# Performance work log

Hardware: AMD Instinct MI355X
Metric: run time of the kernel (lower is better)

Reference implementation:

```python
import jax, jax.numpy as jnp
import numpy as np

B, T, C, H = 16, 2048, 1024, 64

def setup_inputs() -> dict:
    key = jax.random.key(0)
    kx, kq, kk, kv = jax.random.split(key, 4)
    s = 0.02
    return {
        "x": jax.random.normal(kx, (B, T, C), dtype=jnp.float32),
        "Wq": jax.random.normal(kq, (C, H), dtype=jnp.float32) * s,
        "Wk": jax.random.normal(kk, (C, H), dtype=jnp.float32) * s,
        "Wv": jax.random.normal(kv, (C, H), dtype=jnp.float32) * s,
    }

def reference(x, Wq, Wk, Wv):
    Bc, Tc, Cc = x.shape
    q = x @ Wq  # [B,T,H]
    k = x @ Wk  # [B,T,H]
    v = x @ Wv  # [B,T,H]
    # NOTE: original scales by n_embed^{-0.5} (C), not head_size^{-0.5}
    wei = jnp.einsum("bth,bsh->bts", q, k) * (Cc ** -0.5)  # [B,T,T]
    causal = jnp.tril(jnp.ones((Tc, Tc), dtype=bool))
    wei = jnp.where(causal, wei, -jnp.inf)
    wei = jax.nn.softmax(wei, axis=-1)
    # dropout is identity in eval mode
    out = jnp.einsum("bts,bsh->bth", wei, v)  # [B,T,H]
    return out
```

## Files before the change

kernel.cpp:

```cpp
#include <hip/hip_runtime.h>

typedef __attribute__((ext_vector_type(8))) short short8;
typedef __attribute__((ext_vector_type(4))) float float4v;

__device__ inline short f2bf(float f) {
    union { float f; unsigned int u; } c; c.f = f;
    unsigned int u = c.u;
    unsigned int r = (u + 0x7fffu + ((u >> 16) & 1u)) >> 16;
    return (short)r;
}

__global__ __launch_bounds__(256) void wconv_kernel(
    const float* __restrict__ Wq, const float* __restrict__ Wk,
    const float* __restrict__ Wv, short* __restrict__ Wt)
{
    const int n = blockIdx.x;
    const float* W = (n < 64) ? Wq : (n < 128) ? Wk : Wv;
    const int c = n & 63;
#pragma unroll
    for (int i = 0; i < 4; i++) {
        int k = threadIdx.x + i * 256;
        Wt[n * 1024 + k] = f2bf(W[(size_t)k * 64 + c]);
    }
}

#define QSTR 72

__global__ __launch_bounds__(256) void qkv_kernel(
    const float* __restrict__ x, const short* __restrict__ Wt,
    short* __restrict__ qo, short* __restrict__ ko, short* __restrict__ vT)
{
    __shared__ short As[64 * QSTR];
    __shared__ short Bs[192 * QSTR];

    const int tid  = threadIdx.x;
    const int wave = tid >> 6, lane = tid & 63;
    const int quad = lane >> 4, l16 = lane & 15;
    const int m0   = blockIdx.x * 64;

    float4v acc[12];
#pragma unroll
    for (int i = 0; i < 12; i++) acc[i] = (float4v)0.0f;

    const int arow = tid >> 2;
    const int acol = (tid & 3) * 16;

    for (int kc = 0; kc < 1024; kc += 64) {
        __syncthreads();
        {
            const float* src = &x[(size_t)(m0 + arow) * 1024 + kc + acol];
            float4 a0 = ((const float4*)src)[0];
            float4 a1 = ((const float4*)src)[1];
            float4 a2 = ((const float4*)src)[2];
            float4 a3 = ((const float4*)src)[3];
            short8 v0, v1;
            v0[0]=f2bf(a0.x); v0[1]=f2bf(a0.y); v0[2]=f2bf(a0.z); v0[3]=f2bf(a0.w);
            v0[4]=f2bf(a1.x); v0[5]=f2bf(a1.y); v0[6]=f2bf(a1.z); v0[7]=f2bf(a1.w);
            v1[0]=f2bf(a2.x); v1[1]=f2bf(a2.y); v1[2]=f2bf(a2.z); v1[3]=f2bf(a2.w);
            v1[4]=f2bf(a3.x); v1[5]=f2bf(a3.y); v1[6]=f2bf(a3.z); v1[7]=f2bf(a3.w);
            *(short8*)&As[arow * QSTR + acol]     = v0;
            *(short8*)&As[arow * QSTR + acol + 8] = v1;
        }
#pragma unroll
        for (int i = 0; i < 6; i++) {
            int c  = tid + i * 256;
            int n  = c >> 3;
            int k8 = (c & 7) * 8;
            *(short8*)&Bs[n * QSTR + k8] =
                *(const short8*)&Wt[n * 1024 + kc + k8];
        }
        __syncthreads();
#pragma unroll
        for (int kc2 = 0; kc2 < 2; kc2++) {
            short8 af = *(const short8*)&As[(wave*16 + l16) * QSTR + kc2*32 + quad*8];
#pragma unroll
            for (int nt = 0; nt < 12; nt++) {
                short8 bf = *(const short8*)&Bs[(nt*16 + l16) * QSTR + kc2*32 + quad*8];
                acc[nt] = __builtin_amdgcn_mfma_f32_16x16x32_bf16(af, bf, acc[nt], 0, 0, 0);
            }
        }
    }
#pragma unroll
    for (int nt = 0; nt < 8; nt++) {
        short* dst = (nt < 4) ? qo : ko;
        int h = (nt & 3) * 16 + l16;
#pragma unroll
        for (int r = 0; r < 4; r++) {
            int row = m0 + wave*16 + quad*4 + r;
            dst[(size_t)row * 64 + h] = f2bf(acc[nt][r]);
        }
    }
#pragma unroll
    for (int nt = 8; nt < 12; nt++) {
        int h = (nt & 3) * 16 + l16;
#pragma unroll
        for (int r = 0; r < 4; r++) {
            int row = m0 + wave*16 + quad*4 + r;
            int bb = row >> 11, tt = row & 2047;
            vT[((size_t)bb * 64 + h) * 2048 + tt] = f2bf(acc[nt][r]);
        }
    }
}

#define DSTR 72
#define SCALE_LOG2E 0.04508422132f

__global__ __launch_bounds__(256) void attn_kernel(
    const short* __restrict__ q, const short* __restrict__ k,
    const short* __restrict__ vT, float* __restrict__ out)
{
    __shared__ short Ks [64 * DSTR];
    __shared__ short VsT[64 * DSTR];
    __shared__ short Ps [64 * DSTR];

    const int tid  = threadIdx.x;
    const int wave = tid >> 6, lane = tid & 63;
    const int quad = lane >> 4, l16 = lane & 15;
    const int b  = blockIdx.x >> 5;
    const int qt = blockIdx.x & 31;

    const short* kb  = k  + (size_t)b * 2048 * 64;
    const short* vTb = vT + (size_t)b * 64 * 2048;

    const short* qrow = q + ((size_t)b * 2048 + qt*64 + wave*16 + l16) * 64;
    short8 qf0 = *(const short8*)&qrow[quad*8];
    short8 qf1 = *(const short8*)&qrow[32 + quad*8];

    float4v oacc[4];
#pragma unroll
    for (int t = 0; t < 4; t++) oacc[t] = (float4v)0.0f;
    float l_i[4] = {0.f, 0.f, 0.f, 0.f};

    const int tg = qt*64 + wave*16 + quad*4;

    for (int j = 0; j <= qt; j++) {
        __syncthreads();
#pragma unroll
        for (int i = 0; i < 2; i++) {
            int c = tid + i * 256;
            int s = c >> 3, d8 = (c & 7) * 8;
            *(short8*)&Ks[s * DSTR + d8] =
                *(const short8*)&kb[(size_t)(j*64 + s) * 64 + d8];
        }
#pragma unroll
        for (int i = 0; i < 2; i++) {
            int c = tid + i * 256;
            int d = c >> 3, s8 = (c & 7) * 8;
            *(short8*)&VsT[d * DSTR + s8] =
                *(const short8*)&vTb[(size_t)d * 2048 + j*64 + s8];
        }
        __syncthreads();

        float4v sacc[4];
#pragma unroll
        for (int t = 0; t < 4; t++) sacc[t] = (float4v)0.0f;
#pragma unroll
        for (int t = 0; t < 4; t++) {
            short8 bf0 = *(const short8*)&Ks[(t*16 + l16) * DSTR + quad*8];
            short8 bf1 = *(const short8*)&Ks[(t*16 + l16) * DSTR + 32 + quad*8];
            sacc[t] = __builtin_amdgcn_mfma_f32_16x16x32_bf16(qf0, bf0, sacc[t], 0, 0, 0);
            sacc[t] = __builtin_amdgcn_mfma_f32_16x16x32_bf16(qf1, bf1, sacc[t], 0, 0, 0);
        }
        if (j == qt) {
#pragma unroll
            for (int t = 0; t < 4; t++) {
                int sg = j*64 + t*16 + l16;
#pragma unroll
                for (int r = 0; r < 4; r++) {
                    float p = exp2f(sacc[t][r] * SCALE_LOG2E);
                    if (sg > tg + r) p = 0.0f;
                    sacc[t][r] = p;
                    l_i[r] += p;
                }
            }
        } else {
#pragma unroll
            for (int t = 0; t < 4; t++)
#pragma unroll
                for (int r = 0; r < 4; r++) {
                    float p = exp2f(sacc[t][r] * SCALE_LOG2E);
                    sacc[t][r] = p;
                    l_i[r] += p;
                }
        }
#pragma unroll
        for (int t = 0; t < 4; t++)
#pragma unroll
            for (int r = 0; r < 4; r++)
                Ps[(wave*16 + quad*4 + r) * DSTR + t*16 + l16] = f2bf(sacc[t][r]);
#pragma unroll
        for (int kc = 0; kc < 2; kc++) {
            short8 af = *(const short8*)&Ps[(wave*16 + l16) * DSTR + kc*32 + quad*8];
#pragma unroll
            for (int t = 0; t < 4; t++) {
                short8 bf = *(const short8*)&VsT[(t*16 + l16) * DSTR + kc*32 + quad*8];
                oacc[t] = __builtin_amdgcn_mfma_f32_16x16x32_bf16(af, bf, oacc[t], 0, 0, 0);
            }
        }
    }
#pragma unroll
    for (int off = 1; off < 16; off <<= 1)
#pragma unroll
        for (int r = 0; r < 4; r++)
            l_i[r] += __shfl_xor(l_i[r], off, 64);
#pragma unroll
    for (int r = 0; r < 4; r++) {
        float inv = 1.0f / l_i[r];
        int row = qt*64 + wave*16 + quad*4 + r;
#pragma unroll
        for (int t = 0; t < 4; t++)
            out[((size_t)b * 2048 + row) * 64 + t*16 + l16] = oacc[t][r] * inv;
    }
}

extern "C" void kernel_launch(void* const* d_in, const int* in_sizes, int n_in,
                              void* d_out, int out_size, void* d_ws, size_t ws_size,
                              hipStream_t stream)
{
    const float* x  = (const float*)d_in[0];
    const float* Wq = (const float*)d_in[1];
    const float* Wk = (const float*)d_in[2];
    const float* Wv = (const float*)d_in[3];

    short* qw = (short*)d_ws;
    short* kw = qw + (size_t)32768 * 64;
    short* vT = kw + (size_t)32768 * 64;
    short* Wt = vT + (size_t)32768 * 64;
    float* out = (float*)d_out;

    hipLaunchKernelGGL(wconv_kernel, dim3(192), dim3(256), 0, stream,
                       Wq, Wk, Wv, Wt);
    hipLaunchKernelGGL(qkv_kernel, dim3(512), dim3(256), 0, stream,
                       x, Wt, qw, kw, vT);
    hipLaunchKernelGGL(attn_kernel, dim3(512), dim3(256), 0, stream,
                       qw, kw, vT, out);
}
```

Baseline: 303.2 us.

## Rework QKV projection tiling, transpose weights via LDS, reorder attention blocks

The weight conversion kernel now transposes through shared memory so both its global reads and writes are coalesced. The QKV projection drops shared-memory staging. Each wave loads its x fragments and bf16 weight fragments straight from global memory, with 32-row blocks and a 1024-block grid, which removes barriers but gives up LDS reuse of x across waves. Attention launches the long causal query tiles first to balance the triangular workload, and the P tile stride is padded to change the LDS bank pattern.

```diff
diff --git a/kernel.cpp b/kernel.cpp
--- a/kernel.cpp
+++ b/kernel.cpp
@@ -14,95 +14,98 @@
     const float* __restrict__ Wq, const float* __restrict__ Wk,
     const float* __restrict__ Wv, short* __restrict__ Wt)
 {
-    const int n = blockIdx.x;
-    const float* W = (n < 64) ? Wq : (n < 128) ? Wk : Wv;
-    const int c = n & 63;
+    __shared__ short Ls[64 * 72];
+    const int w  = blockIdx.x >> 4;
+    const int k0 = (blockIdx.x & 15) * 64;
+    const float* W = (w == 0) ? Wq : (w == 1) ? Wk : Wv;
+    const int tid = threadIdx.x;
+
 #pragma unroll
     for (int i = 0; i < 4; i++) {
-        int k = threadIdx.x + i * 256;
-        Wt[n * 1024 + k] = f2bf(W[(size_t)k * 64 + c]);
-    }
-}
-
-#define QSTR 72
+        int kk = (tid >> 4) + i * 16;
+        int c4 = (tid & 15) * 4;
+        float4 v = *(const float4*)&W[(size_t)(k0 + kk) * 64 + c4];
+        Ls[kk * 72 + c4 + 0] = f2bf(v.x);
+        Ls[kk * 72 + c4 + 1] = f2bf(v.y);
+        Ls[kk * 72 + c4 + 2] = f2bf(v.z);
+        Ls[kk * 72 + c4 + 3] = f2bf(v.w);
+    }
+    __syncthreads();
+    const int n  = tid >> 2;
+    const int k8 = (tid & 3) * 16;
+    short8 o0, o1;
+#pragma unroll
+    for (int j = 0; j < 8; j++) o0[j] = Ls[(k8 + j) * 72 + n];
+#pragma unroll
+    for (int j = 0; j < 8; j++) o1[j] = Ls[(k8 + 8 + j) * 72 + n];
+    short* dst = &Wt[(size_t)(w * 64 + n) * 1024 + k0 + k8];
+    *(short8*)dst = o0;
+    *(short8*)(dst + 8) = o1;
+}
 
 __global__ __launch_bounds__(256) void qkv_kernel(
     const float* __restrict__ x, const short* __restrict__ Wt,
     short* __restrict__ qo, short* __restrict__ ko, short* __restrict__ vT)
 {
-    __shared__ short As[64 * QSTR];
-    __shared__ short Bs[192 * QSTR];
-
     const int tid  = threadIdx.x;
     const int wave = tid >> 6, lane = tid & 63;
     const int quad = lane >> 4, l16 = lane & 15;
-    const int m0   = blockIdx.x * 64;
-
-    float4v acc[12];
-#pragma unroll
-    for (int i = 0; i < 12; i++) acc[i] = (float4v)0.0f;
-
-    const int arow = tid >> 2;
-    const int acol = (tid & 3) * 16;
-
-    for (int kc = 0; kc < 1024; kc += 64) {
-        __syncthreads();
-        {
-            const float* src = &x[(size_t)(m0 + arow) * 1024 + kc + acol];
-            float4 a0 = ((const float4*)src)[0];
-            float4 a1 = ((const float4*)src)[1];
-            float4 a2 = ((const float4*)src)[2];
-            float4 a3 = ((const float4*)src)[3];
-            short8 v0, v1;
-            v0[0]=f2bf(a0.x); v0[1]=f2bf(a0.y); v0[2]=f2bf(a0.z); v0[3]=f2bf(a0.w);
-            v0[4]=f2bf(a1.x); v0[5]=f2bf(a1.y); v0[6]=f2bf(a1.z); v0[7]=f2bf(a1.w);
-            v1[0]=f2bf(a2.x); v1[1]=f2bf(a2.y); v1[2]=f2bf(a2.z); v1[3]=f2bf(a2.w);
-            v1[4]=f2bf(a3.x); v1[5]=f2bf(a3.y); v1[6]=f2bf(a3.z); v1[7]=f2bf(a3.w);
-            *(short8*)&As[arow * QSTR + acol]     = v0;
-            *(short8*)&As[arow * QSTR + acol + 8] = v1;
-        }
-#pragma unroll
-        for (int i = 0; i < 6; i++) {
-            int c  = tid + i * 256;
-            int n  = c >> 3;
-            int k8 = (c & 7) * 8;
-            *(short8*)&Bs[n * QSTR + k8] =
-                *(const short8*)&Wt[n * 1024 + kc + k8];
-        }
-        __syncthreads();
-#pragma unroll
-        for (int kc2 = 0; kc2 < 2; kc2++) {
-            short8 af = *(const short8*)&As[(wave*16 + l16) * QSTR + kc2*32 + quad*8];
-#pragma unroll
-            for (int nt = 0; nt < 12; nt++) {
-                short8 bf = *(const short8*)&Bs[(nt*16 + l16) * QSTR + kc2*32 + quad*8];
-                acc[nt] = __builtin_amdgcn_mfma_f32_16x16x32_bf16(af, bf, acc[nt], 0, 0, 0);
+    const int m0   = blockIdx.x * 32;
+    const int n0   = wave * 48;
+
+    float4v acc[2][3];
+#pragma unroll
+    for (int mf = 0; mf < 2; mf++)
+#pragma unroll
+        for (int nt = 0; nt < 3; nt++) acc[mf][nt] = (float4v)0.0f;
+
+    const float* ap0 = &x[(size_t)(m0 + l16) * 1024 + quad * 8];
+    const float* ap1 = ap0 + (size_t)16 * 1024;
+    const short* bp  = &Wt[(size_t)(n0 + l16) * 1024 + quad * 8];
+
+#pragma unroll 2
+    for (int k = 0; k < 1024; k += 32) {
+        short8 af[2];
+#pragma unroll
+        for (int mf = 0; mf < 2; mf++) {
+            const float* ap = (mf == 0) ? ap0 : ap1;
+            float4 x0 = *(const float4*)(ap + k);
+            float4 x1 = *(const float4*)(ap + k + 4);
+            short8 a;
+            a[0]=f2bf(x0.x); a[1]=f2bf(x0.y); a[2]=f2bf(x0.z); a[3]=f2bf(x0.w);
+            a[4]=f2bf(x1.x); a[5]=f2bf(x1.y); a[6]=f2bf(x1.z); a[7]=f2bf(x1.w);
+            af[mf] = a;
+        }
+#pragma unroll
+        for (int nt = 0; nt < 3; nt++) {
+            short8 bf = *(const short8*)(bp + (size_t)nt * 16 * 1024 + k);
+            acc[0][nt] = __builtin_amdgcn_mfma_f32_16x16x32_bf16(af[0], bf, acc[0][nt], 0, 0, 0);
+            acc[1][nt] = __builtin_amdgcn_mfma_f32_16x16x32_bf16(af[1], bf, acc[1][nt], 0, 0, 0);
+        }
+    }
+#pragma unroll
+    for (int mf = 0; mf < 2; mf++) {
+        int row0 = m0 + mf * 16 + quad * 4;
+#pragma unroll
+        for (int nt = 0; nt < 3; nt++) {
+            int g = n0 + nt * 16 + l16;
+#pragma unroll
+            for (int r = 0; r < 4; r++) {
+                short val = f2bf(acc[mf][nt][r]);
+                int row = row0 + r;
+                if (g < 64)       qo[(size_t)row * 64 + g] = val;
+                else if (g < 128) ko[(size_t)row * 64 + (g - 64)] = val;
+                else {
+                    int bb = row >> 11, tt = row & 2047;
+                    vT[((size_t)bb * 64 + (g - 128)) * 2048 + tt] = val;
+                }
             }
         }
     }
-#pragma unroll
-    for (int nt = 0; nt < 8; nt++) {
-        short* dst = (nt < 4) ? qo : ko;
-        int h = (nt & 3) * 16 + l16;
-#pragma unroll
-        for (int r = 0; r < 4; r++) {
-            int row = m0 + wave*16 + quad*4 + r;
-            dst[(size_t)row * 64 + h] = f2bf(acc[nt][r]);
-        }
-    }
-#pragma unroll
-    for (int nt = 8; nt < 12; nt++) {
-        int h = (nt & 3) * 16 + l16;
-#pragma unroll
-        for (int r = 0; r < 4; r++) {
-            int row = m0 + wave*16 + quad*4 + r;
-            int bb = row >> 11, tt = row & 2047;
-            vT[((size_t)bb * 64 + h) * 2048 + tt] = f2bf(acc[nt][r]);
-        }
-    }
 }
 
 #define DSTR 72
+#define PSTR 76
 #define SCALE_LOG2E 0.04508422132f
 
 __global__ __launch_bounds__(256) void attn_kernel(
@@ -111,13 +114,15 @@
 {
     __shared__ short Ks [64 * DSTR];
     __shared__ short VsT[64 * DSTR];
-    __shared__ short Ps [64 * DSTR];
+    __shared__ short Ps [64 * PSTR];
 
     const int tid  = threadIdx.x;
     const int wave = tid >> 6, lane = tid & 63;
     const int quad = lane >> 4, l16 = lane & 15;
-    const int b  = blockIdx.x >> 5;
-    const int qt = blockIdx.x & 31;
+
+    int b, qt;
+    if (blockIdx.x < 256) { b = blockIdx.x >> 4; qt = 16 + (blockIdx.x & 15); }
+    else { int t = blockIdx.x - 256; b = t >> 4; qt = 15 - (t & 15); }
 
     const short* kb  = k  + (size_t)b * 2048 * 64;
     const short* vTb = vT + (size_t)b * 64 * 2048;
@@ -187,10 +192,10 @@
         for (int t = 0; t < 4; t++)
 #pragma unroll
             for (int r = 0; r < 4; r++)
-                Ps[(wave*16 + quad*4 + r) * DSTR + t*16 + l16] = f2bf(sacc[t][r]);
+                Ps[(wave*16 + quad*4 + r) * PSTR + t*16 + l16] = f2bf(sacc[t][r]);
 #pragma unroll
         for (int kc = 0; kc < 2; kc++) {
-            short8 af = *(const short8*)&Ps[(wave*16 + l16) * DSTR + kc*32 + quad*8];
+            short8 af = *(const short8*)&Ps[(wave*16 + l16) * PSTR + kc*32 + quad*8];
 #pragma unroll
             for (int t = 0; t < 4; t++) {
                 short8 bf = *(const short8*)&VsT[(t*16 + l16) * DSTR + kc*32 + quad*8];
@@ -228,9 +233,9 @@
     short* Wt = vT + (size_t)32768 * 64;
     float* out = (float*)d_out;
 
-    hipLaunchKernelGGL(wconv_kernel, dim3(192), dim3(256), 0, stream,
+    hipLaunchKernelGGL(wconv_kernel, dim3(48), dim3(256), 0, stream,
                        Wq, Wk, Wv, Wt);
-    hipLaunchKernelGGL(qkv_kernel, dim3(512), dim3(256), 0, stream,
+    hipLaunchKernelGGL(qkv_kernel, dim3(1024), dim3(256), 0, stream,
                        x, Wt, qw, kw, vT);
     hipLaunchKernelGGL(attn_kernel, dim3(512), dim3(256), 0, stream,
                        qw, kw, vT, out);
```

Result: slower. 328.3 us (+8.3%).
